# Optimization experiments

Measured on AMD Instinct MI355X. Metric: run time of the kernel, lower is better.

Reference implementation:

```python
import jax, jax.numpy as jnp
import numpy as np

S = 100                     # MC weight samples
B = 128                     # batch
CONV1 = (100, 20, 1, 5, 5)  # (S, Cout, Cin, kh, kw)
CONV2 = (100, 50, 20, 5, 5)
AFF1 = (100, 500, 800)      # (S, out, in)
AFF2 = (100, 10, 500)
W_OFF = np.cumsum([0, 500, 25000, 400000, 5000])
B_OFF = np.cumsum([0, 20, 50, 500, 10])
NW, NB = 430500, 580


def _softplus(r):
    return jnp.log1p(jnp.exp(r))  # sigma_T(rho) = log(1 + exp(rho))


def _conv(h, w, b):
    # h: (B, S or 1, Cin, H, W); w: (S, Cout, Cin, kh, kw); b: (S, Cout)
    def one(xs, ws):  # xs: (B,Cin,H,W), ws: (Cout,Cin,kh,kw)
        return jax.lax.conv_general_dilated(xs, ws, (1, 1), 'VALID')
    if h.shape[1] == 1:  # shared input broadcast over samples (first layer)
        out = jax.vmap(one, in_axes=(None, 0), out_axes=1)(h[:, 0], w)
    else:
        out = jax.vmap(one, in_axes=(1, 0), out_axes=1)(h, w)
    return out + b[None, :, :, None, None]  # (B,S,Cout,H',W')


def _maxpool(h):  # 2x2 stride-2 over trailing spatial dims
    return jax.lax.reduce_window(h, -jnp.inf, jax.lax.max,
                                 (1, 1, 1, 2, 2), (1, 1, 1, 2, 2), 'VALID')


def setup_inputs() -> dict:
    key = jax.random.key(0)
    ks = jax.random.split(key, 4)
    x = jax.random.normal(ks[0], (B, 1, 28, 28), dtype=jnp.float32)
    e = jax.random.normal(ks[1], (S, NW + NB), dtype=jnp.float32)
    mu_w = jax.random.normal(ks[2], (NW,), dtype=jnp.float32) * 0.05
    rho_w = jnp.ones((NW,), dtype=jnp.float32) * 0.5
    mu_b = jax.random.normal(ks[3], (NB,), dtype=jnp.float32) * 0.05
    rho_b = jnp.ones((NB,), dtype=jnp.float32) * 0.5
    return {"x": x, "e": e, "mu_w": mu_w, "rho_w": rho_w,
            "mu_b": mu_b, "rho_b": rho_b}


def reference(x, e, mu_w, rho_w, mu_b, rho_b):
    # reparameterized per-sample weights: (S, NW) and (S, NB)
    w = mu_w + _softplus(rho_w) * e[:, :NW]
    b = mu_b + _softplus(rho_b) * e[:, NW:]

    h = x[:, None]  # (B,1,1,28,28): singleton MC dim broadcasts
    # conv1 + relu + pool
    h = _conv(h, w[:, W_OFF[0]:W_OFF[1]].reshape(CONV1), b[:, B_OFF[0]:B_OFF[1]])
    h = _maxpool(jax.nn.relu(h))                     # (B,S,20,12,12)
    # conv2 + relu + pool
    h = _conv(h, w[:, W_OFF[1]:W_OFF[2]].reshape(CONV2), b[:, B_OFF[1]:B_OFF[2]])
    h = _maxpool(jax.nn.relu(h))                     # (B,S,50,4,4)
    h = h.reshape(h.shape[0], h.shape[1], -1)        # (B,S,800)
    # aff1 + relu
    w3 = w[:, W_OFF[2]:W_OFF[3]].reshape(AFF1)
    h = jax.nn.relu(jnp.einsum('bsi,soi->bso', h, w3) + b[None, :, B_OFF[2]:B_OFF[3]])
    # aff2 + log_softmax
    w4 = w[:, W_OFF[3]:W_OFF[4]].reshape(AFF2)
    h = jnp.einsum('bsi,soi->bso', h, w4) + b[None, :, B_OFF[3]:B_OFF[4]]
    h = jax.nn.log_softmax(h, axis=-1)               # (B,S,10)
    return h.mean(axis=1)                            # eval path: mean over MC samples
```

## Files before the change

kernel.cpp:

```cpp
#include <hip/hip_runtime.h>
#include <math.h>

#define Sn 100
#define Bn 128
#define NWc 430500
#define EWc 431080

typedef __attribute__((ext_vector_type(8)))  short bhalf8;
typedef __attribute__((ext_vector_type(16))) float fx16;

__device__ __forceinline__ float sp_f(float r){
    return fmaxf(r, 0.f) + log1pf(__expf(-fabsf(r)));
}
__device__ __forceinline__ ushort bfr(float f){
    union { float f; uint u; } c; c.f = f;
    uint r = (c.u + 0x7FFFu + ((c.u >> 16) & 1u)) >> 16;
    return (ushort)r;
}

__global__ void k0_gen(const float* __restrict__ e, const float* __restrict__ mu_w,
                       const float* __restrict__ rho_w, const float* __restrict__ mu_b,
                       const float* __restrict__ rho_b,
                       float* __restrict__ w1, ushort* __restrict__ w2r,
                       float* __restrict__ w4, float* __restrict__ ball){
    const int per = 31080;
    int idx = blockIdx.x * blockDim.x + threadIdx.x;
    if (idx >= Sn * per) return;
    int s = idx / per, j = idx % per;
    if (j < 500){
        float v = mu_w[j] + sp_f(rho_w[j]) * e[s*EWc + j];
        w1[s*500 + j] = v;
    } else if (j < 25500){
        int g = j;
        float v = mu_w[g] + sp_f(rho_w[g]) * e[s*EWc + g];
        int j2 = j - 500;
        int oc = j2 / 500, rem = j2 % 500;
        int ic = rem / 25, kk = rem % 25;
        w2r[s*51200 + (kk*64 + oc)*32 + ic] = bfr(v);
    } else if (j < 30500){
        int g = 425500 + (j - 25500);
        float v = mu_w[g] + sp_f(rho_w[g]) * e[s*EWc + g];
        w4[s*5000 + (j - 25500)] = v;
    } else {
        int k = j - 30500;
        float v = mu_b[k] + sp_f(rho_b[k]) * e[s*EWc + NWc + k];
        ball[s*580 + k] = v;
    }
}

__global__ __launch_bounds__(256, 2) void k1_conv1(const float* __restrict__ x,
        const float* __restrict__ w1, const float* __restrict__ ball,
        ushort* __restrict__ h1p){
    __shared__ __align__(16) float xs[784];
    __shared__ __align__(16) float w1s[500];
    __shared__ float b1s[20];
    __shared__ __align__(16) ushort ots[2880];
    int bid = blockIdx.x;
    int s = bid / Bn, b = bid % Bn;
    int tid = threadIdx.x;
    for (int i = tid; i < 784; i += 256) xs[i] = x[b*784 + i];
    for (int i = tid; i < 500; i += 256) w1s[i] = w1[s*500 + i];
    if (tid < 20) b1s[tid] = ball[s*580 + tid];
    __syncthreads();
    if (tid < 240){
        int c = tid / 12, y = tid % 12;

        float acc0[24], acc1[24];
        #pragma unroll
        for (int i = 0; i < 24; ++i){ acc0[i] = 0.f; acc1[i] = 0.f; }

        #pragma unroll
        for (int ky = 0; ky < 5; ++ky){
            float rlo[28], rhi[28];
            const float* plo = &xs[(2*y + ky) * 28];
            const float* phi = &xs[(2*y + ky + 1) * 28];
            #pragma unroll
            for (int cc = 0; cc < 28; cc += 4){
                float4 v0 = *(const float4*)(plo + cc);
                rlo[cc] = v0.x; rlo[cc+1] = v0.y; rlo[cc+2] = v0.z; rlo[cc+3] = v0.w;
                float4 v1 = *(const float4*)(phi + cc);
                rhi[cc] = v1.x; rhi[cc+1] = v1.y; rhi[cc+2] = v1.z; rhi[cc+3] = v1.w;
            }
            #pragma unroll
            for (int kx = 0; kx < 5; ++kx){
                float wv = w1s[c*25 + ky*5 + kx];
                #pragma unroll
                for (int cx = 0; cx < 24; ++cx){
                    acc0[cx] = fmaf(rlo[cx + kx], wv, acc0[cx]);
                    acc1[cx] = fmaf(rhi[cx + kx], wv, acc1[cx]);
                }
            }
        }
        float bias = b1s[c];
        #pragma unroll
        for (int px = 0; px < 12; ++px){
            float m = fmaxf(fmaxf(acc0[2*px], acc0[2*px+1]),
                            fmaxf(acc1[2*px], acc1[2*px+1]));
            ots[(y*12 + px)*20 + c] = bfr(fmaxf(m + bias, 0.f));
        }
    }
    __syncthreads();
    const uint* o32 = (const uint*)ots;
    uint* g32 = (uint*)(h1p + (s*Bn + b)*2880);
    for (int j = tid; j < 1440; j += 256) g32[j] = o32[j];
}

#define ICS 40
__global__ __launch_bounds__(256, 3) void k2_mfma(const ushort* __restrict__ h1p,
        const ushort* __restrict__ w2r, const float* __restrict__ ball,
        ushort* __restrict__ h2p){
    __shared__ __align__(16) ushort img[4*144*ICS];
    __shared__ __align__(16) ushort Bs[64*ICS];
    int bid = blockIdx.x;
    int s = bid >> 5, g = bid & 31;
    int tid = threadIdx.x;
    const uint* g32 = (const uint*)(h1p + (size_t)(s*Bn + g*4)*2880);
    uint* l32 = (uint*)img;
    for (int j = tid; j < 5760; j += 256){
        int im = j / 1440, r = j - im*1440;
        int p = r / 10, u = r - p*10;
        l32[im*2880 + p*20 + u] = g32[j];
    }
    for (int j = tid; j < 3456; j += 256){
        int im = j / 864, r = j - im*864;
        int p = r / 6, u = 10 + (r - p*6);
        l32[im*2880 + p*20 + u] = 0u;
    }
    int wv = tid >> 6, l = tid & 63;
    int l31 = l & 31, q = l >> 5;
    const ushort* imgw = img + wv*5760;
    int pixb0 = ((l31      ) >> 3)*12 + (l31 & 7);
    int pixb1 = ((l31 + 32 ) >> 3)*12 + (l31 & 7);
    fx16 acc00 = (fx16)0.f, acc01 = (fx16)0.f, acc10 = (fx16)0.f, acc11 = (fx16)0.f;

    for (int kk = 0; kk < 25; ++kk){
        __syncthreads();
        {
            uint4 v = ((const uint4*)(w2r + (size_t)(s*25 + kk)*2048))[tid];
            *(uint4*)&Bs[(tid>>2)*ICS + (tid&3)*8] = v;
        }
        __syncthreads();
        int ky = kk / 5, kx = kk - ky*5;
        int poff = ky*12 + kx;
        #pragma unroll
        for (int ics = 0; ics < 2; ++ics){
            bhalf8 a0 = *(const bhalf8*)(imgw + (pixb0 + poff)*ICS + ics*16 + q*8);
            bhalf8 a1 = *(const bhalf8*)(imgw + (pixb1 + poff)*ICS + ics*16 + q*8);
            bhalf8 b0 = *(const bhalf8*)(Bs + (l31     )*ICS + ics*16 + q*8);
            bhalf8 b1 = *(const bhalf8*)(Bs + (l31 + 32)*ICS + ics*16 + q*8);
            acc00 = __builtin_amdgcn_mfma_f32_32x32x16_bf16(a0, b0, acc00, 0, 0, 0);
            acc01 = __builtin_amdgcn_mfma_f32_32x32x16_bf16(a0, b1, acc01, 0, 0, 0);
            acc10 = __builtin_amdgcn_mfma_f32_32x32x16_bf16(a1, b0, acc10, 0, 0, 0);
            acc11 = __builtin_amdgcn_mfma_f32_32x32x16_bf16(a1, b1, acc11, 0, 0, 0);
        }
    }
    int b = g*4 + wv;
    ushort* dst = h2p + (size_t)(s*Bn + b)*800;
    #pragma unroll
    for (int nt = 0; nt < 2; ++nt){
        int oc = nt*32 + l31;
        if (oc >= 50) continue;
        float bias = ball[s*580 + 20 + oc];
        #pragma unroll
        for (int mt = 0; mt < 2; ++mt){
            fx16 a;
            if (nt == 0) a = mt ? acc10 : acc00;
            else         a = mt ? acc11 : acc01;
            #pragma unroll
            for (int gp = 0; gp < 2; ++gp){
                float p0 = fmaxf(fmaxf(a[8*gp+0], a[8*gp+1]), fmaxf(a[8*gp+4], a[8*gp+5]));
                float p1 = fmaxf(fmaxf(a[8*gp+2], a[8*gp+3]), fmaxf(a[8*gp+6], a[8*gp+7]));
                p0 = fmaxf(p0 + bias, 0.f);
                p1 = fmaxf(p1 + bias, 0.f);
                int py = mt*2 + gp, px0 = 2*q;
                uint pk = (uint)bfr(p0) | ((uint)bfr(p1) << 16);
                *(uint*)(dst + oc*16 + py*4 + px0) = pk;
            }
        }
    }
}

__global__ __launch_bounds__(256, 4) void k3_mfma(const ushort* __restrict__ h2p,
        const float* __restrict__ e, const float* __restrict__ mu_w,
        const float* __restrict__ rho_w, const float* __restrict__ ball,
        float* __restrict__ h3){
    __shared__ __align__(16) ushort As[128*ICS];
    __shared__ __align__(16) ushort Bsh[64*ICS];
    int bid = blockIdx.x;
    int s = bid >> 3, nblk = bid & 7;
    int o0 = nblk * 64;
    int tid = threadIdx.x;
    const float* mu3  = mu_w  + 25500;
    const float* rho3 = rho_w + 25500;
    const float* e3   = e + (size_t)s*EWc + 25500;
    int wv = tid >> 6, l = tid & 63, l31 = l & 31, q = l >> 5;
    int wm = wv >> 1, wn = wv & 1;
    fx16 acc0 = (fx16)0.f, acc1 = (fx16)0.f;
    int sb = tid >> 1, sh = tid & 1;
    int so = tid >> 2, sk = (tid & 3)*8;
    int og = o0 + so;

    for (int k0 = 0; k0 < 800; k0 += 32){
        __syncthreads();
        {
            const uint4* src = (const uint4*)(h2p + (size_t)(s*Bn + sb)*800 + k0 + sh*16);
            uint4 v0 = src[0], v1 = src[1];
            *(uint4*)&As[sb*ICS + sh*16]     = v0;
            *(uint4*)&As[sb*ICS + sh*16 + 8] = v1;
        }
        {
            ushort tmp[8];
            if (og < 500){
                int gg = og*800 + k0 + sk;
                #pragma unroll
                for (int j = 0; j < 8; ++j){
                    float v = mu3[gg+j] + sp_f(rho3[gg+j]) * e3[gg+j];
                    tmp[j] = bfr(v);
                }
            } else {
                #pragma unroll
                for (int j = 0; j < 8; ++j) tmp[j] = 0;
            }
            *(uint4*)&Bsh[so*ICS + sk] = *(const uint4*)tmp;
        }
        __syncthreads();
        #pragma unroll
        for (int ks = 0; ks < 2; ++ks){
            bhalf8 a0 = *(const bhalf8*)&As[(wm*64      + l31)*ICS + ks*16 + q*8];
            bhalf8 a1 = *(const bhalf8*)&As[(wm*64 + 32 + l31)*ICS + ks*16 + q*8];
            bhalf8 bb = *(const bhalf8*)&Bsh[(wn*32 + l31)*ICS + ks*16 + q*8];
            acc0 = __builtin_amdgcn_mfma_f32_32x32x16_bf16(a0, bb, acc0, 0, 0, 0);
            acc1 = __builtin_amdgcn_mfma_f32_32x32x16_bf16(a1, bb, acc1, 0, 0, 0);
        }
    }
    int o = o0 + wn*32 + l31;
    if (o < 500){
        float bias = ball[s*580 + 70 + o];
        #pragma unroll
        for (int mt = 0; mt < 2; ++mt){
            fx16 a = mt ? acc1 : acc0;
            #pragma unroll
            for (int reg = 0; reg < 16; ++reg){
                int row = (reg & 3) + 8*(reg >> 2) + 4*q;
                int b = wm*64 + mt*32 + row;
                h3[(size_t)(s*Bn + b)*500 + o] = fmaxf(a[reg] + bias, 0.f);
            }
        }
    }
}

__global__ __launch_bounds__(256) void k4a(const float* __restrict__ h3,
        const float* __restrict__ w4, const float* __restrict__ ball,
        float* __restrict__ lsw){
    int wv = threadIdx.x >> 6, lane = threadIdx.x & 63;
    int p = blockIdx.x*4 + wv;
    int s = p / Bn;
    const float* hp = &h3[(size_t)p*500];
    const float* wp = &w4[(size_t)s*5000];
    float part[10];
    #pragma unroll
    for (int o = 0; o < 10; ++o) part[o] = 0.f;
    for (int i = lane; i < 500; i += 64){
        float hv = hp[i];
        #pragma unroll
        for (int o = 0; o < 10; ++o)
            part[o] = fmaf(hv, wp[o*500 + i], part[o]);
    }
    #pragma unroll
    for (int o = 0; o < 10; ++o){
        #pragma unroll
        for (int d = 1; d < 64; d <<= 1)
            part[o] += __shfl_xor(part[o], d);
    }
    float v[10]; float m = -INFINITY;
    #pragma unroll
    for (int o = 0; o < 10; ++o){
        v[o] = part[o] + ball[s*580 + 570 + o];
        m = fmaxf(m, v[o]);
    }
    float sum = 0.f;
    #pragma unroll
    for (int o = 0; o < 10; ++o) sum += __expf(v[o] - m);
    float lse = m + __logf(sum);
    if (lane == 0){
        #pragma unroll
        for (int o = 0; o < 10; ++o) lsw[p*10 + o] = v[o] - lse;
    }
}

__global__ void k4b(const float* __restrict__ lsw, float* __restrict__ outp){
    int j = blockIdx.x * blockDim.x + threadIdx.x;
    if (j >= Bn*10) return;
    int b = j / 10, o = j % 10;
    float acc = 0.f;
    for (int s2 = 0; s2 < Sn; ++s2) acc += lsw[(s2*Bn + b)*10 + o];
    outp[j] = acc * (1.f / (float)Sn);
}

extern "C" void kernel_launch(void* const* d_in, const int* in_sizes, int n_in,
                              void* d_out, int out_size, void* d_ws, size_t ws_size,
                              hipStream_t stream){
    const float* x     = (const float*)d_in[0];
    const float* e     = (const float*)d_in[1];
    const float* mu_w  = (const float*)d_in[2];
    const float* rho_w = (const float*)d_in[3];
    const float* mu_b  = (const float*)d_in[4];
    const float* rho_b = (const float*)d_in[5];
    float* ws   = (float*)d_ws;
    float* w1   = ws;
    float* w4   = w1 + 50000;
    float* ball = w4 + 500000;
    float* h3   = ball + 58000;
    float* lsw  = h3 + 6400000;
    ushort* h1p = (ushort*)(lsw + 128000);
    ushort* h2p = h1p + 36864000;
    ushort* w2r = h2p + 10240000;
    float* outp = (float*)d_out;

    hipMemsetAsync(w2r, 0, (size_t)Sn*51200*2, stream);
    k0_gen  <<<(Sn*31080 + 255)/256, 256, 0, stream>>>(e, mu_w, rho_w, mu_b, rho_b, w1, w2r, w4, ball);
    k1_conv1<<<Sn*Bn, 256, 0, stream>>>(x, w1, ball, h1p);
    k2_mfma <<<Sn*32, 256, 0, stream>>>(h1p, w2r, ball, h2p);
    k3_mfma <<<Sn*8, 256, 0, stream>>>(h2p, e, mu_w, rho_w, ball, h3);
    k4a     <<<3200, 256, 0, stream>>>(h3, w4, ball, lsw);
    k4b     <<<(Bn*10 + 255)/256, 256, 0, stream>>>(lsw, outp);
}
```

Baseline: 617.0 us.

## Precompute softplus once and prefetch next k-tile in aff1 MFMA kernel

Adds a small kernel that evaluates softplus(rho) once per parameter instead of once per MC sample, so weight generation becomes a single FMA. In the aff1 MFMA kernel, the next k-slice of activations and mu/sp/eps is loaded into registers with float4 loads while the current tile's MFMAs run. The launch-bounds occupancy hint is also relaxed. The cost is an extra kernel launch, extra register pressure from the prefetch buffers, and reading a precomputed sp array instead of rho.

Result: faster. 566.5 us (-8.2%).

```diff
diff --git a/kernel.cpp b/kernel.cpp
--- a/kernel.cpp
+++ b/kernel.cpp
@@ -18,9 +18,15 @@
     return (ushort)r;
 }
 
+__global__ void k00_sp(const float* __restrict__ rho_w, const float* __restrict__ rho_b,
+                       float* __restrict__ sp_all){
+    int i = blockIdx.x * blockDim.x + threadIdx.x;
+    if (i < NWc)      sp_all[i] = sp_f(rho_w[i]);
+    else if (i < EWc) sp_all[i] = sp_f(rho_b[i - NWc]);
+}
+
 __global__ void k0_gen(const float* __restrict__ e, const float* __restrict__ mu_w,
-                       const float* __restrict__ rho_w, const float* __restrict__ mu_b,
-                       const float* __restrict__ rho_b,
+                       const float* __restrict__ sp_all, const float* __restrict__ mu_b,
                        float* __restrict__ w1, ushort* __restrict__ w2r,
                        float* __restrict__ w4, float* __restrict__ ball){
     const int per = 31080;
@@ -28,22 +34,22 @@
     if (idx >= Sn * per) return;
     int s = idx / per, j = idx % per;
     if (j < 500){
-        float v = mu_w[j] + sp_f(rho_w[j]) * e[s*EWc + j];
+        float v = fmaf(sp_all[j], e[s*EWc + j], mu_w[j]);
         w1[s*500 + j] = v;
     } else if (j < 25500){
         int g = j;
-        float v = mu_w[g] + sp_f(rho_w[g]) * e[s*EWc + g];
+        float v = fmaf(sp_all[g], e[s*EWc + g], mu_w[g]);
         int j2 = j - 500;
         int oc = j2 / 500, rem = j2 % 500;
         int ic = rem / 25, kk = rem % 25;
         w2r[s*51200 + (kk*64 + oc)*32 + ic] = bfr(v);
     } else if (j < 30500){
         int g = 425500 + (j - 25500);
-        float v = mu_w[g] + sp_f(rho_w[g]) * e[s*EWc + g];
+        float v = fmaf(sp_all[g], e[s*EWc + g], mu_w[g]);
         w4[s*5000 + (j - 25500)] = v;
     } else {
         int k = j - 30500;
-        float v = mu_b[k] + sp_f(rho_b[k]) * e[s*EWc + NWc + k];
+        float v = fmaf(sp_all[NWc + k], e[s*EWc + NWc + k], mu_b[k]);
         ball[s*580 + k] = v;
     }
 }
@@ -180,9 +186,9 @@
     }
 }
 
-__global__ __launch_bounds__(256, 4) void k3_mfma(const ushort* __restrict__ h2p,
+__global__ __launch_bounds__(256) void k3_mfma(const ushort* __restrict__ h2p,
         const float* __restrict__ e, const float* __restrict__ mu_w,
-        const float* __restrict__ rho_w, const float* __restrict__ ball,
+        const float* __restrict__ sp_all, const float* __restrict__ ball,
         float* __restrict__ h3){
     __shared__ __align__(16) ushort As[128*ICS];
     __shared__ __align__(16) ushort Bsh[64*ICS];
@@ -190,40 +196,58 @@
     int s = bid >> 3, nblk = bid & 7;
     int o0 = nblk * 64;
     int tid = threadIdx.x;
-    const float* mu3  = mu_w  + 25500;
-    const float* rho3 = rho_w + 25500;
-    const float* e3   = e + (size_t)s*EWc + 25500;
     int wv = tid >> 6, l = tid & 63, l31 = l & 31, q = l >> 5;
     int wm = wv >> 1, wn = wv & 1;
     fx16 acc0 = (fx16)0.f, acc1 = (fx16)0.f;
     int sb = tid >> 1, sh = tid & 1;
     int so = tid >> 2, sk = (tid & 3)*8;
     int og = o0 + so;
+    bool bvalid = og < 500;
+    const float* mp = mu_w   + 25500 + og*800 + sk;
+    const float* pp = sp_all + 25500 + og*800 + sk;
+    const float* ep = e + (size_t)s*EWc + 25500 + og*800 + sk;
+    const ushort* ap = h2p + (size_t)(s*Bn + sb)*800 + sh*16;
+
+    uint4 ar0, ar1;
+    float4 mva, mvb, sva, svb, eva, evb;
+    ar0 = ((const uint4*)ap)[0]; ar1 = ((const uint4*)ap)[1];
+    if (bvalid){
+        mva = *(const float4*)(mp);   mvb = *(const float4*)(mp + 4);
+        sva = *(const float4*)(pp);   svb = *(const float4*)(pp + 4);
+        eva = *(const float4*)(ep);   evb = *(const float4*)(ep + 4);
+    }
 
     for (int k0 = 0; k0 < 800; k0 += 32){
         __syncthreads();
-        {
-            const uint4* src = (const uint4*)(h2p + (size_t)(s*Bn + sb)*800 + k0 + sh*16);
-            uint4 v0 = src[0], v1 = src[1];
-            *(uint4*)&As[sb*ICS + sh*16]     = v0;
-            *(uint4*)&As[sb*ICS + sh*16 + 8] = v1;
-        }
+        *(uint4*)&As[sb*ICS + sh*16]     = ar0;
+        *(uint4*)&As[sb*ICS + sh*16 + 8] = ar1;
         {
             ushort tmp[8];
-            if (og < 500){
-                int gg = og*800 + k0 + sk;
-                #pragma unroll
-                for (int j = 0; j < 8; ++j){
-                    float v = mu3[gg+j] + sp_f(rho3[gg+j]) * e3[gg+j];
-                    tmp[j] = bfr(v);
-                }
+            if (bvalid){
+                tmp[0] = bfr(fmaf(sva.x, eva.x, mva.x));
+                tmp[1] = bfr(fmaf(sva.y, eva.y, mva.y));
+                tmp[2] = bfr(fmaf(sva.z, eva.z, mva.z));
+                tmp[3] = bfr(fmaf(sva.w, eva.w, mva.w));
+                tmp[4] = bfr(fmaf(svb.x, evb.x, mvb.x));
+                tmp[5] = bfr(fmaf(svb.y, evb.y, mvb.y));
+                tmp[6] = bfr(fmaf(svb.z, evb.z, mvb.z));
+                tmp[7] = bfr(fmaf(svb.w, evb.w, mvb.w));
             } else {
                 #pragma unroll
-                for (int j = 0; j < 8; ++j) tmp[j] = 0;
+                for (int j2 = 0; j2 < 8; ++j2) tmp[j2] = 0;
             }
             *(uint4*)&Bsh[so*ICS + sk] = *(const uint4*)tmp;
         }
         __syncthreads();
+        int kn = k0 + 32;
+        if (kn < 800){
+            ar0 = ((const uint4*)(ap + kn))[0]; ar1 = ((const uint4*)(ap + kn))[1];
+            if (bvalid){
+                mva = *(const float4*)(mp + kn);  mvb = *(const float4*)(mp + kn + 4);
+                sva = *(const float4*)(pp + kn);  svb = *(const float4*)(pp + kn + 4);
+                eva = *(const float4*)(ep + kn);  evb = *(const float4*)(ep + kn + 4);
+            }
+        }
         #pragma unroll
         for (int ks = 0; ks < 2; ++ks){
             bhalf8 a0 = *(const bhalf8*)&As[(wm*64      + l31)*ICS + ks*16 + q*8];
@@ -307,21 +331,23 @@
     const float* mu_b  = (const float*)d_in[4];
     const float* rho_b = (const float*)d_in[5];
     float* ws   = (float*)d_ws;
-    float* w1   = ws;
-    float* w4   = w1 + 50000;
-    float* ball = w4 + 500000;
-    float* h3   = ball + 58000;
-    float* lsw  = h3 + 6400000;
-    ushort* h1p = (ushort*)(lsw + 128000);
+    float* w1     = ws;
+    float* w4     = w1 + 50000;
+    float* ball   = w4 + 500000;
+    float* h3     = ball + 58000;
+    float* lsw    = h3 + 6400000;
+    float* sp_all = lsw + 128000;
+    ushort* h1p = (ushort*)(sp_all + 431080);
     ushort* h2p = h1p + 36864000;
     ushort* w2r = h2p + 10240000;
     float* outp = (float*)d_out;
 
     hipMemsetAsync(w2r, 0, (size_t)Sn*51200*2, stream);
-    k0_gen  <<<(Sn*31080 + 255)/256, 256, 0, stream>>>(e, mu_w, rho_w, mu_b, rho_b, w1, w2r, w4, ball);
+    k00_sp  <<<(EWc + 255)/256, 256, 0, stream>>>(rho_w, rho_b, sp_all);
+    k0_gen  <<<(Sn*31080 + 255)/256, 256, 0, stream>>>(e, mu_w, sp_all, mu_b, w1, w2r, w4, ball);
     k1_conv1<<<Sn*Bn, 256, 0, stream>>>(x, w1, ball, h1p);
     k2_mfma <<<Sn*32, 256, 0, stream>>>(h1p, w2r, ball, h2p);
-    k3_mfma <<<Sn*8, 256, 0, stream>>>(h2p, e, mu_w, rho_w, ball, h3);
+    k3_mfma <<<Sn*8, 256, 0, stream>>>(h2p, e, mu_w, sp_all, ball, h3);
     k4a     <<<3200, 256, 0, stream>>>(h3, w4, ball, lsw);
     k4b     <<<(Bn*10 + 255)/256, 256, 0, stream>>>(lsw, outp);
 }
```
